# Performance work log

Hardware: AMD Instinct MI355X
Metric: run time of the kernel (lower is better)

## Reference

```python
import jax, jax.numpy as jnp
import numpy as np

B, N, D, H = 256, 196, 384, 1536  # batch, patches, dim, mlp hidden


def fake_quant(w, bits):
    """Symmetric per-tensor uniform fake quantization with straight-through estimator."""
    qmax = 2.0 ** (bits - 1) - 1.0
    scale = jnp.maximum(jnp.max(jnp.abs(w)) / qmax, 1e-8)
    q = jnp.clip(jnp.round(w / scale), -qmax, qmax) * scale
    return w + jax.lax.stop_gradient(q - w)


def setup_inputs() -> dict:
    key = jax.random.key(0)
    ks = jax.random.split(key, 8)
    return {
        "x": jax.random.normal(ks[0], (B, N, D), jnp.float32),
        "alpha1": jnp.ones((D,), jnp.float32),
        "beta1": jnp.zeros((D,), jnp.float32),
        "W_attn": jax.random.normal(ks[1], (N, N), jnp.float32) * (1.0 / np.sqrt(N)),
        "b_attn": jnp.zeros((N,), jnp.float32),
        "gamma1": jax.random.uniform(ks[2], (D,), jnp.float32) * 0.1,
        "alpha2": jnp.ones((D,), jnp.float32),
        "beta2": jnp.zeros((D,), jnp.float32),
        "W1": jax.random.normal(ks[3], (H, D), jnp.float32) * (1.0 / np.sqrt(D)),
        "b1": jnp.zeros((H,), jnp.float32),
        "W2": jax.random.normal(ks[4], (D, H), jnp.float32) * (1.0 / np.sqrt(H)),
        "b2": jnp.zeros((D,), jnp.float32),
        "gamma2": jax.random.uniform(ks[5], (D,), jnp.float32) * 0.1,
        "bits": 8,
    }


def reference(x, alpha1, beta1, W_attn, b_attn, gamma1,
              alpha2, beta2, W1, b1, W2, b2, gamma2, bits):
    # --- token-mixing branch ---
    org = x
    h = alpha1 * x + beta1                                   # Aff norm1, [B,N,D]
    # transpose(1,2) -> [B,D,N]; Linear(N,N); transpose back == einsum over patch dim
    Wq = fake_quant(W_attn, bits)
    h = jnp.einsum('bnd,mn->bmd', h, Wq) + b_attn[:, None]   # [B,N,D], bias per patch
    x = gamma1 * h + org                                     # layerscale + residual
    # --- channel-mixing branch ---
    org = x
    h = alpha2 * x + beta2                                   # Aff norm2
    h = jax.nn.gelu(h @ fake_quant(W1, bits).T + b1)         # [B,N,H]
    h = h @ fake_quant(W2, bits).T + b2                      # [B,N,D]
    return gamma2 * h + org
```

## Files before the change

kernel.cpp:

```cpp
#include <hip/hip_runtime.h>
#include <hip/hip_bf16.h>
#include <stdint.h>

#define Bb 256
#define Nn 196
#define Dd 384
#define Hh 1536
#define NPAD 224
#define MPAD 256
#define TTOT (Bb*Nn)
#define XLD 232
#define TK 64
#define HS 128

typedef __attribute__((ext_vector_type(8))) __bf16 bf16x8;
typedef __attribute__((ext_vector_type(4))) float f32x4;

#define GLD16(gp, lp) __builtin_amdgcn_global_load_lds( \
    (const __attribute__((address_space(1))) void*)(gp), \
    (__attribute__((address_space(3))) void*)(lp), 16, 0, 0)

#define MFMA16(a, b, c) __builtin_amdgcn_mfma_f32_16x16x32_bf16((a), (b), (c), 0, 0, 0)

__device__ __forceinline__ ushort f2bf(float f){
  union { float f; unsigned u; } v; v.f = f;
  unsigned r = v.u + 0x7FFFu + ((v.u >> 16) & 1u);
  return (ushort)(r >> 16);
}

__global__ void absmax3_k(const float* __restrict__ wa, const float* __restrict__ w1,
                          const float* __restrict__ w2, unsigned* __restrict__ out){
  int which = blockIdx.y;
  const float* w = which == 0 ? wa : (which == 1 ? w1 : w2);
  int n = which == 0 ? Nn*Nn : Hh*Dd;
  float m = 0.f;
  for (int i = blockIdx.x*blockDim.x + threadIdx.x; i < n; i += gridDim.x*blockDim.x)
    m = fmaxf(m, fabsf(w[i]));
  #pragma unroll
  for (int o = 32; o >= 1; o >>= 1) m = fmaxf(m, __shfl_xor(m, o));
  __shared__ float sm[4];
  if ((threadIdx.x & 63) == 0) sm[threadIdx.x >> 6] = m;
  __syncthreads();
  if (threadIdx.x == 0){
    float mm = fmaxf(fmaxf(sm[0], sm[1]), fmaxf(sm[2], sm[3]));
    atomicMax(out + which, __float_as_uint(mm));
  }
}

__global__ void quant_attn_k(const float* __restrict__ W, const unsigned* __restrict__ amax,
                             const int* __restrict__ bitsp, ushort* __restrict__ Wq){
  int idx = blockIdx.x*256 + threadIdx.x;
  int m = idx / NPAD, n = idx - m*NPAD;
  float qmax = (float)((1 << (bitsp[0]-1)) - 1);
  float s = fmaxf(__uint_as_float(amax[0]) / qmax, 1e-8f);
  float v = 0.f;
  if (m < Nn && n < Nn){
    float q = fminf(fmaxf(rintf(W[m*Nn + n] / s), -qmax), qmax);
    v = q * s;
  }
  Wq[idx] = f2bf(v);
}

__global__ void quant_k(const float* __restrict__ W, int n, const unsigned* __restrict__ amax,
                        const int* __restrict__ bitsp, ushort* __restrict__ Wq){
  int idx = blockIdx.x*256 + threadIdx.x;
  if (idx >= n) return;
  float qmax = (float)((1 << (bitsp[0]-1)) - 1);
  float s = fmaxf(__uint_as_float(amax[0]) / qmax, 1e-8f);
  float q = fminf(fmaxf(rintf(W[idx] / s), -qmax), qmax);
  Wq[idx] = f2bf(q * s);
}

__device__ __forceinline__ void stage_tile(const ushort* __restrict__ src, long ld, int k0,
                                           ushort* dst){
  const int tid = threadIdx.x;
  const long row = tid >> 2;
  const int  c8  = (tid & 3) * 8;
  GLD16(src + row*ld + k0 + c8,        dst + tid*8);
  GLD16(src + (row+64)*ld + k0 + c8,   dst + 2048 + tid*8);
}

__global__ __launch_bounds__(256) void gemm1_k(const ushort* __restrict__ Wq,
    const float* __restrict__ x,
    const float* __restrict__ alpha1, const float* __restrict__ beta1,
    const float* __restrict__ b_attn, const float* __restrict__ gamma1,
    const float* __restrict__ alpha2, const float* __restrict__ beta2,
    float* __restrict__ x1, ushort* __restrict__ hn2){
  __shared__ ushort Xs[128*XLD];
  __shared__ ushort BufAs[8192];
  const int tid = threadIdx.x;
  const int b = blockIdx.y, dt = blockIdx.x, d0 = dt*128;

  {
    float* buf = (float*)BufAs;
    const int dme = tid & 127;
    const float a1 = alpha1[d0 + dme], be1 = beta1[d0 + dme];
    for (int p = 0; p < 7; p++){
      __syncthreads();
      #pragma unroll
      for (int c = 0; c < 4; c++){
        int nn = p*32 + c*8 + (tid >> 5);
        int ncl = nn < Nn ? nn : Nn - 1;
        GLD16(x + ((long)b*Nn + ncl)*Dd + d0 + (tid & 31)*4,
              (char*)BufAs + c*4096 + tid*16);
      }
      __syncthreads();
      for (int g = tid >> 7; g < 4; g += 2){
        int n0 = g*8;
        ushort o[8];
        #pragma unroll
        for (int t = 0; t < 8; t++){
          int na = p*32 + n0 + t;
          float val = (na < Nn) ? fmaf(a1, buf[(n0 + t)*128 + dme], be1) : 0.f;
          o[t] = f2bf(val);
        }
        *(int4*)&Xs[dme*XLD + p*32 + n0] = *(int4*)o;
      }
    }
  }

  const int lane = tid & 63;
  const int wr = (tid >> 7) & 1, wc = (tid >> 6) & 1;
  const int arow = lane & 15, koff = (lane >> 4)*8;
  ushort* As = BufAs;
  for (int mt = 0; mt < 2; mt++){
    f32x4 acc[4][4] = {};
    const ushort* Wt = Wq + (long)mt*128*NPAD;
    for (int k0 = 0; k0 < NPAD; k0 += 32){
      __syncthreads();
      stage_tile(Wt, NPAD, k0, As);
      __syncthreads();
      bf16x8 ag[4], bg[4];
      #pragma unroll
      for (int i=0;i<4;i++){
        ag[i] = *(const bf16x8*)&As[(wr*64 + i*16 + arow)*32 + koff];
        bg[i] = *(const bf16x8*)&Xs[(wc*64 + i*16 + arow)*XLD + k0 + koff];
      }
      #pragma unroll
      for (int i=0;i<4;i++)
        #pragma unroll
        for (int j=0;j<4;j++)
          acc[i][j] = MFMA16(ag[i], bg[j], acc[i][j]);
    }
    #pragma unroll
    for (int i=0;i<4;i++){
      #pragma unroll
      for (int j=0;j<4;j++){
        int d = d0 + wc*64 + j*16 + (lane & 15);
        float g1 = gamma1[d], a2 = alpha2[d], b2v = beta2[d];
        #pragma unroll
        for (int r=0;r<4;r++){
          int m = mt*128 + wr*64 + i*16 + (lane >> 4)*4 + r;
          if (m < Nn){
            long idx = ((long)b*Nn + m)*Dd + d;
            float o = fmaf(g1, acc[i][j][r] + b_attn[m], x[idx]);
            x1[idx]  = o;
            hn2[idx] = f2bf(fmaf(a2, o, b2v));
          }
        }
      }
    }
  }
}


__device__ __forceinline__ void stage_a(const ushort* __restrict__ hn2, long t0, int k0,
                                        const ushort* __restrict__ W1q, int hs,
                                        ushort* As, ushort* W1s){
  const int tid = threadIdx.x;
  const int w = tid >> 6, lane = tid & 63;
  const int srcc = (((lane & 7) ^ ((lane >> 3) & 7))) * 8;
  const int rowa = w*8 + (lane >> 3);
  GLD16(hn2 + (t0 + rowa)*Dd + k0 + srcc,        As + (w*64 + lane)*8);
  GLD16(hn2 + (t0 + 32 + rowa)*Dd + k0 + srcc,   As + (256 + w*64 + lane)*8);
  #pragma unroll
  for (int q = 0; q < 4; q++){
    int row = q*32 + rowa;
    GLD16(W1q + ((long)hs*HS + row)*Dd + k0 + srcc, W1s + (q*256 + w*64 + lane)*8);
  }
}

__device__ __forceinline__ void stage_b(const ushort* __restrict__ W2q, int hcol0,
                                        ushort* W2s){
  const int tid = threadIdx.x;
  const int w = tid >> 6, lane = tid & 63;
  const int srcc = ((lane & 3) ^ ((lane >> 3) & 3)) * 8;
  #pragma unroll
  for (int q = 0; q < 6; q++){
    int row = q*64 + w*16 + (lane >> 2);
    GLD16(W2q + (long)row*Hh + hcol0 + srcc, W2s + (q*256 + w*64 + lane)*8);
  }
}

__global__ __launch_bounds__(256, 2) void mlp_k(const ushort* __restrict__ hn2,
    const ushort* __restrict__ W1q, const ushort* __restrict__ W2q,
    const float* __restrict__ b1, const float* __restrict__ b2,
    const float* __restrict__ gamma2, float* __restrict__ out){
  __shared__ ushort SH[36864];
  ushort* const AsP[2] = { SH, SH + 4096 };
  ushort* const Ps     = SH + 4096;
  ushort* const WsP[2] = { SH + 12288, SH + 24576 };

  const int tid  = threadIdx.x;
  const int lane = tid & 63;
  const int wv   = tid >> 6;
  const int arow = lane & 15;
  const int g    = lane >> 4;
  const long t0  = (long)blockIdx.x * TK;

  f32x4 oacc[4][6] = {};

  stage_a(hn2, t0, 0, W1q, 0, AsP[0], WsP[0]);
  __syncthreads();

  for (int hs = 0; hs < 12; hs++){
    f32x4 pacc[4][2] = {};
    #pragma unroll
    for (int ka = 0; ka < 6; ka++){
      const int cur = ka & 1;
      if (ka < 5) stage_a(hn2, t0, (ka+1)*64, W1q, hs, AsP[cur^1], WsP[cur^1]);
      else        stage_b(W2q, hs*HS, WsP[0]);
      const ushort* As  = AsP[cur];
      const ushort* W1s = WsP[cur];
      bf16x8 ag[4][2], bg[2][2];
      #pragma unroll
      for (int i=0;i<4;i++)
        #pragma unroll
        for (int ks=0;ks<2;ks++)
          ag[i][ks] = *(const bf16x8*)&As[(i*16 + arow)*64 + (((ks*4 + g) ^ (arow & 7))*8)];
      #pragma unroll
      for (int j=0;j<2;j++)
        #pragma unroll
        for (int ks=0;ks<2;ks++)
          bg[j][ks] = *(const bf16x8*)&W1s[(wv*32 + j*16 + arow)*64 + (((ks*4 + g) ^ (arow & 7))*8)];
      #pragma unroll
      for (int ks=0;ks<2;ks++)
        #pragma unroll
        for (int i=0;i<4;i++)
          #pragma unroll
          for (int j=0;j<2;j++)
            pacc[i][j] = MFMA16(ag[i][ks], bg[j][ks], pacc[i][j]);
      __syncthreads();
    }
    #pragma unroll
    for (int j=0;j<2;j++){
      int hcol = wv*32 + j*16 + arow;
      float b1v = b1[hs*HS + hcol];
      #pragma unroll
      for (int i=0;i<4;i++){
        #pragma unroll
        for (int r=0;r<4;r++){
          int row = i*16 + g*4 + r;
          float v = pacc[i][j][r] + b1v;
          float u = 0.7978845608028654f * v * fmaf(0.044715f, v*v, 1.f);
          float gl = v / (1.f + __expf(-2.f*u));
          Ps[row*128 + (hcol ^ ((row & 7) << 3))] = f2bf(gl);
        }
      }
    }
    __syncthreads();
    #pragma unroll
    for (int kb = 0; kb < 4; kb++){
      const int cur = kb & 1;
      if (kb < 3)       stage_b(W2q, hs*HS + (kb+1)*32, WsP[cur^1]);
      else if (hs < 11) stage_a(hn2, t0, 0, W1q, hs+1, AsP[0], WsP[0]);
      const ushort* W2s = WsP[cur];
      bf16x8 pa[4], bgb[6];
      #pragma unroll
      for (int i=0;i<4;i++){
        int row = i*16 + arow;
        pa[i] = *(const bf16x8*)&Ps[row*128 + ((kb*32 + g*8) ^ ((row & 7) << 3))];
      }
      #pragma unroll
      for (int j=0;j<6;j++){
        int row = wv*96 + j*16 + arow;
        bgb[j] = *(const bf16x8*)&W2s[row*32 + ((g ^ ((arow >> 1) & 3))*8)];
      }
      #pragma unroll
      for (int i=0;i<4;i++)
        #pragma unroll
        for (int j=0;j<6;j++)
          oacc[i][j] = MFMA16(pa[i], bgb[j], oacc[i][j]);
      __syncthreads();
    }
  }

  #pragma unroll
  for (int i=0;i<4;i++){
    #pragma unroll
    for (int j=0;j<6;j++){
      int d = wv*96 + j*16 + arow;
      float g2 = gamma2[d], b2v = b2[d];
      #pragma unroll
      for (int r=0;r<4;r++){
        long t = t0 + i*16 + g*4 + r;
        long idx = t*Dd + d;
        out[idx] = fmaf(g2, oacc[i][j][r] + b2v, out[idx]);
      }
    }
  }
}

extern "C" void kernel_launch(void* const* d_in, const int* in_sizes, int n_in,
                              void* d_out, int out_size, void* d_ws, size_t ws_size,
                              hipStream_t stream){
  const float* x      = (const float*)d_in[0];
  const float* alpha1 = (const float*)d_in[1];
  const float* beta1  = (const float*)d_in[2];
  const float* W_attn = (const float*)d_in[3];
  const float* b_attn = (const float*)d_in[4];
  const float* gamma1 = (const float*)d_in[5];
  const float* alpha2 = (const float*)d_in[6];
  const float* beta2  = (const float*)d_in[7];
  const float* W1     = (const float*)d_in[8];
  const float* b1     = (const float*)d_in[9];
  const float* W2     = (const float*)d_in[10];
  const float* b2     = (const float*)d_in[11];
  const float* gamma2 = (const float*)d_in[12];
  const int*   bits   = (const int*)d_in[13];

  char* ws = (char*)d_ws;
  unsigned* amax = (unsigned*)ws;
  ushort* Wq   = (ushort*)(ws + 256);
  ushort* W1q  = (ushort*)(ws + 114944);
  ushort* W2q  = (ushort*)(ws + 1294592);
  ushort* hn2  = (ushort*)(ws + 2474240);
  float*  x1   = (float*)d_out;

  hipMemsetAsync(amax, 0, 256, stream);
  absmax3_k<<<dim3(128, 3), 256, 0, stream>>>(W_attn, W1, W2, amax);
  quant_attn_k<<<(MPAD*NPAD)/256, 256, 0, stream>>>(W_attn, amax, bits, Wq);
  quant_k<<<(Hh*Dd)/256, 256, 0, stream>>>(W1, Hh*Dd, amax + 1, bits, W1q);
  quant_k<<<(Hh*Dd)/256, 256, 0, stream>>>(W2, Hh*Dd, amax + 2, bits, W2q);
  gemm1_k<<<dim3(3, Bb), 256, 0, stream>>>(Wq, x, alpha1, beta1, b_attn, gamma1,
                                           alpha2, beta2, x1, hn2);
  mlp_k<<<TTOT/TK, 256, 0, stream>>>(hn2, W1q, W2q, b1, b2, gamma2, (float*)d_out);
}
```

Before: 376.3 us.

## Deepen MLP pipeline with 3-slot LDS ring, 128-token tiles and 512 threads

Reworks the fused MLP kernel to process 128 tokens per block with 8 waves, a three-slot LDS ring buffer and partial vmcnt waits, so global-to-LDS loads run two stages ahead instead of syncing fully after each step. It also caches b1 in LDS, raises wave priority around MFMA bursts, and removes per-k shared-memory staging of Wq in gemm1 by reading Wq directly from global memory. The aim is more reuse of W1 and W2 across tokens and better overlap of loads with compute. The costs are higher LDS use per block, which limits occupancy, and fragile hand-written waitcnt counts.

```diff
diff --git a/kernel.cpp b/kernel.cpp
--- a/kernel.cpp
+++ b/kernel.cpp
@@ -10,7 +10,7 @@
 #define MPAD 256
 #define TTOT (Bb*Nn)
 #define XLD 232
-#define TK 64
+#define TK 128
 #define HS 128
 
 typedef __attribute__((ext_vector_type(8))) __bf16 bf16x8;
@@ -21,6 +21,9 @@
     (__attribute__((address_space(3))) void*)(lp), 16, 0, 0)
 
 #define MFMA16(a, b, c) __builtin_amdgcn_mfma_f32_16x16x32_bf16((a), (b), (c), 0, 0, 0)
+
+#define PHASE_SYNC   asm volatile("s_waitcnt vmcnt(4)\ns_barrier" ::: "memory")
+#define PHASE_SYNC_L asm volatile("s_waitcnt vmcnt(4) lgkmcnt(0)\ns_barrier" ::: "memory")
 
 __device__ __forceinline__ ushort f2bf(float f){
   union { float f; unsigned u; } v; v.f = f;
@@ -71,28 +74,18 @@
   Wq[idx] = f2bf(q * s);
 }
 
-__device__ __forceinline__ void stage_tile(const ushort* __restrict__ src, long ld, int k0,
-                                           ushort* dst){
-  const int tid = threadIdx.x;
-  const long row = tid >> 2;
-  const int  c8  = (tid & 3) * 8;
-  GLD16(src + row*ld + k0 + c8,        dst + tid*8);
-  GLD16(src + (row+64)*ld + k0 + c8,   dst + 2048 + tid*8);
-}
-
-__global__ __launch_bounds__(256) void gemm1_k(const ushort* __restrict__ Wq,
+__global__ __launch_bounds__(256, 2) void gemm1_k(const ushort* __restrict__ Wq,
     const float* __restrict__ x,
     const float* __restrict__ alpha1, const float* __restrict__ beta1,
     const float* __restrict__ b_attn, const float* __restrict__ gamma1,
     const float* __restrict__ alpha2, const float* __restrict__ beta2,
     float* __restrict__ x1, ushort* __restrict__ hn2){
   __shared__ ushort Xs[128*XLD];
-  __shared__ ushort BufAs[8192];
+  __shared__ float  Sbuf[32*128];
   const int tid = threadIdx.x;
   const int b = blockIdx.y, dt = blockIdx.x, d0 = dt*128;
 
   {
-    float* buf = (float*)BufAs;
     const int dme = tid & 127;
     const float a1 = alpha1[d0 + dme], be1 = beta1[d0 + dme];
     for (int p = 0; p < 7; p++){
@@ -102,7 +95,7 @@
         int nn = p*32 + c*8 + (tid >> 5);
         int ncl = nn < Nn ? nn : Nn - 1;
         GLD16(x + ((long)b*Nn + ncl)*Dd + d0 + (tid & 31)*4,
-              (char*)BufAs + c*4096 + tid*16);
+              (char*)Sbuf + c*4096 + tid*16);
       }
       __syncthreads();
       for (int g = tid >> 7; g < 4; g += 2){
@@ -111,30 +104,28 @@
         #pragma unroll
         for (int t = 0; t < 8; t++){
           int na = p*32 + n0 + t;
-          float val = (na < Nn) ? fmaf(a1, buf[(n0 + t)*128 + dme], be1) : 0.f;
+          float val = (na < Nn) ? fmaf(a1, Sbuf[(n0 + t)*128 + dme], be1) : 0.f;
           o[t] = f2bf(val);
         }
         *(int4*)&Xs[dme*XLD + p*32 + n0] = *(int4*)o;
       }
     }
   }
+  __syncthreads();
 
   const int lane = tid & 63;
   const int wr = (tid >> 7) & 1, wc = (tid >> 6) & 1;
   const int arow = lane & 15, koff = (lane >> 4)*8;
-  ushort* As = BufAs;
   for (int mt = 0; mt < 2; mt++){
     f32x4 acc[4][4] = {};
-    const ushort* Wt = Wq + (long)mt*128*NPAD;
-    for (int k0 = 0; k0 < NPAD; k0 += 32){
-      __syncthreads();
-      stage_tile(Wt, NPAD, k0, As);
-      __syncthreads();
+    #pragma unroll
+    for (int k7 = 0; k7 < 7; k7++){
       bf16x8 ag[4], bg[4];
       #pragma unroll
       for (int i=0;i<4;i++){
-        ag[i] = *(const bf16x8*)&As[(wr*64 + i*16 + arow)*32 + koff];
-        bg[i] = *(const bf16x8*)&Xs[(wc*64 + i*16 + arow)*XLD + k0 + koff];
+        int row = mt*128 + wr*64 + i*16 + arow;
+        ag[i] = *(const bf16x8*)&Wq[row*NPAD + k7*32 + koff];
+        bg[i] = *(const bf16x8*)&Xs[(wc*64 + i*16 + arow)*XLD + k7*32 + koff];
       }
       #pragma unroll
       for (int i=0;i<4;i++)
@@ -164,75 +155,83 @@
 }
 
 
-__device__ __forceinline__ void stage_a(const ushort* __restrict__ hn2, long t0, int k0,
-                                        const ushort* __restrict__ W1q, int hs,
-                                        ushort* As, ushort* W1s){
+__device__ __forceinline__ void stage_A(const ushort* __restrict__ hn2t,
+                                        const ushort* __restrict__ W1q, int hs, int ka,
+                                        ushort* slot){
   const int tid = threadIdx.x;
-  const int w = tid >> 6, lane = tid & 63;
-  const int srcc = (((lane & 7) ^ ((lane >> 3) & 7))) * 8;
-  const int rowa = w*8 + (lane >> 3);
-  GLD16(hn2 + (t0 + rowa)*Dd + k0 + srcc,        As + (w*64 + lane)*8);
-  GLD16(hn2 + (t0 + 32 + rowa)*Dd + k0 + srcc,   As + (256 + w*64 + lane)*8);
-  #pragma unroll
-  for (int q = 0; q < 4; q++){
-    int row = q*32 + rowa;
-    GLD16(W1q + ((long)hs*HS + row)*Dd + k0 + srcc, W1s + (q*256 + w*64 + lane)*8);
-  }
-}
-
-__device__ __forceinline__ void stage_b(const ushort* __restrict__ W2q, int hcol0,
-                                        ushort* W2s){
+  const int r0 = tid >> 3;
+  const int cs = ((tid & 7) ^ (r0 & 7)) * 8;
+  const int k0 = ka*64;
+  const ushort* w1 = W1q + (long)hs*HS*Dd + k0;
+  GLD16(hn2t + (long)r0*Dd + k0 + cs,        slot + tid*8);
+  GLD16(hn2t + (long)(r0+64)*Dd + k0 + cs,   slot + 4096 + tid*8);
+  GLD16(w1 + (long)r0*Dd + cs,               slot + 8192 + tid*8);
+  GLD16(w1 + (long)(r0+64)*Dd + cs,          slot + 12288 + tid*8);
+}
+
+__device__ __forceinline__ void stage_B(const ushort* __restrict__ W2q, int hs, int kb,
+                                        ushort* slot){
   const int tid = threadIdx.x;
-  const int w = tid >> 6, lane = tid & 63;
-  const int srcc = ((lane & 3) ^ ((lane >> 3) & 3)) * 8;
-  #pragma unroll
-  for (int q = 0; q < 6; q++){
-    int row = q*64 + w*16 + (lane >> 2);
-    GLD16(W2q + (long)row*Hh + hcol0 + srcc, W2s + (q*256 + w*64 + lane)*8);
-  }
-}
-
-__global__ __launch_bounds__(256, 2) void mlp_k(const ushort* __restrict__ hn2,
+  const int r = tid >> 2;
+  const int cs = ((tid & 3) ^ ((r >> 1) & 3)) * 8;
+  const ushort* w2 = W2q + hs*HS + kb*32;
+  GLD16(w2 + (long)r*Hh + cs,          slot + tid*8);
+  GLD16(w2 + (long)(r+128)*Hh + cs,    slot + 4096 + tid*8);
+  GLD16(w2 + (long)(r+256)*Hh + cs,    slot + 8192 + tid*8);
+  GLD16(w2 + (long)(r+384)*Hh + cs,    slot + 12288 + tid*8);
+}
+
+__global__ __launch_bounds__(512, 2) void mlp_k(const ushort* __restrict__ hn2,
     const ushort* __restrict__ W1q, const ushort* __restrict__ W2q,
     const float* __restrict__ b1, const float* __restrict__ b2,
     const float* __restrict__ gamma2, float* __restrict__ out){
-  __shared__ ushort SH[36864];
-  ushort* const AsP[2] = { SH, SH + 4096 };
-  ushort* const Ps     = SH + 4096;
-  ushort* const WsP[2] = { SH + 12288, SH + 24576 };
+  __shared__ ushort RING[3*16384];
+  __shared__ ushort Ps[TK*HS];
+  __shared__ float  b1s[Hh];
 
   const int tid  = threadIdx.x;
   const int lane = tid & 63;
   const int wv   = tid >> 6;
+  const int wt   = wv >> 2;
+  const int wh   = wv & 3;
   const int arow = lane & 15;
+  const int a7   = arow & 7;
   const int g    = lane >> 4;
   const long t0  = (long)blockIdx.x * TK;
+  const ushort* hn2t = hn2 + t0*Dd;
+
+  if (tid < 384) *(float4*)&b1s[tid*4] = *(const float4*)&b1[tid*4];
+
+  stage_A(hn2t, W1q, 0, 0, RING);
+  stage_A(hn2t, W1q, 0, 1, RING + 16384);
+  __syncthreads();
 
   f32x4 oacc[4][6] = {};
-
-  stage_a(hn2, t0, 0, W1q, 0, AsP[0], WsP[0]);
-  __syncthreads();
-
-  for (int hs = 0; hs < 12; hs++){
+  int cs = 0, ns = 2;
+
+  for (int hs = 0; hs < 12; ++hs){
+    const int hsn = (hs < 11) ? hs + 1 : 11;
     f32x4 pacc[4][2] = {};
     #pragma unroll
-    for (int ka = 0; ka < 6; ka++){
-      const int cur = ka & 1;
-      if (ka < 5) stage_a(hn2, t0, (ka+1)*64, W1q, hs, AsP[cur^1], WsP[cur^1]);
-      else        stage_b(W2q, hs*HS, WsP[0]);
-      const ushort* As  = AsP[cur];
-      const ushort* W1s = WsP[cur];
+    for (int p = 0; p < 6; ++p){
+      PHASE_SYNC;
+      ushort* st = RING + ns*16384;
+      if (p < 4) stage_A(hn2t, W1q, hs, p+2, st);
+      else       stage_B(W2q, hs, p-4, st);
+      const ushort* Asl = RING + cs*16384;
+      const ushort* W1l = Asl + 8192;
       bf16x8 ag[4][2], bg[2][2];
       #pragma unroll
-      for (int i=0;i<4;i++)
-        #pragma unroll
-        for (int ks=0;ks<2;ks++)
-          ag[i][ks] = *(const bf16x8*)&As[(i*16 + arow)*64 + (((ks*4 + g) ^ (arow & 7))*8)];
-      #pragma unroll
-      for (int j=0;j<2;j++)
-        #pragma unroll
-        for (int ks=0;ks<2;ks++)
-          bg[j][ks] = *(const bf16x8*)&W1s[(wv*32 + j*16 + arow)*64 + (((ks*4 + g) ^ (arow & 7))*8)];
+      for (int ks=0; ks<2; ks++){
+        const int cu8 = ((ks*4 + g) ^ a7) * 8;
+        #pragma unroll
+        for (int i=0;i<4;i++)
+          ag[i][ks] = *(const bf16x8*)&Asl[(wt*64 + i*16 + arow)*64 + cu8];
+        #pragma unroll
+        for (int j=0;j<2;j++)
+          bg[j][ks] = *(const bf16x8*)&W1l[(wh*32 + j*16 + arow)*64 + cu8];
+      }
+      __builtin_amdgcn_s_setprio(1);
       #pragma unroll
       for (int ks=0;ks<2;ks++)
         #pragma unroll
@@ -240,60 +239,64 @@
           #pragma unroll
           for (int j=0;j<2;j++)
             pacc[i][j] = MFMA16(ag[i][ks], bg[j][ks], pacc[i][j]);
-      __syncthreads();
+      __builtin_amdgcn_s_setprio(0);
+      cs = cs==2?0:cs+1; ns = ns==2?0:ns+1;
     }
     #pragma unroll
     for (int j=0;j<2;j++){
-      int hcol = wv*32 + j*16 + arow;
-      float b1v = b1[hs*HS + hcol];
+      int hcol = wh*32 + j*16 + arow;
+      float b1v = b1s[hs*HS + hcol];
       #pragma unroll
       for (int i=0;i<4;i++){
         #pragma unroll
         for (int r=0;r<4;r++){
-          int row = i*16 + g*4 + r;
+          int row = wt*64 + i*16 + g*4 + r;
           float v = pacc[i][j][r] + b1v;
           float u = 0.7978845608028654f * v * fmaf(0.044715f, v*v, 1.f);
           float gl = v / (1.f + __expf(-2.f*u));
-          Ps[row*128 + (hcol ^ ((row & 7) << 3))] = f2bf(gl);
+          Ps[row*HS + (hcol ^ ((row & 7) << 3))] = f2bf(gl);
         }
       }
     }
-    __syncthreads();
-    #pragma unroll
-    for (int kb = 0; kb < 4; kb++){
-      const int cur = kb & 1;
-      if (kb < 3)       stage_b(W2q, hs*HS + (kb+1)*32, WsP[cur^1]);
-      else if (hs < 11) stage_a(hn2, t0, 0, W1q, hs+1, AsP[0], WsP[0]);
-      const ushort* W2s = WsP[cur];
+    #pragma unroll
+    for (int p = 6; p < 10; ++p){
+      if (p == 6) { PHASE_SYNC_L; } else { PHASE_SYNC; }
+      ushort* st = RING + ns*16384;
+      if (p < 8) stage_B(W2q, hs, p-4, st);
+      else       stage_A(hn2t, W1q, hsn, p-8, st);
+      const ushort* W2l = RING + cs*16384;
+      const int kb = p - 6;
       bf16x8 pa[4], bgb[6];
       #pragma unroll
       for (int i=0;i<4;i++){
-        int row = i*16 + arow;
-        pa[i] = *(const bf16x8*)&Ps[row*128 + ((kb*32 + g*8) ^ ((row & 7) << 3))];
-      }
-      #pragma unroll
-      for (int j=0;j<6;j++){
-        int row = wv*96 + j*16 + arow;
-        bgb[j] = *(const bf16x8*)&W2s[row*32 + ((g ^ ((arow >> 1) & 3))*8)];
-      }
+        int row = wt*64 + i*16 + arow;
+        pa[i] = *(const bf16x8*)&Ps[row*HS + ((kb*32 + g*8) ^ (a7 << 3))];
+      }
+      const int u8 = (g ^ ((arow >> 1) & 3)) * 8;
+      #pragma unroll
+      for (int j=0;j<6;j++)
+        bgb[j] = *(const bf16x8*)&W2l[(wh*96 + j*16 + arow)*32 + u8];
+      __builtin_amdgcn_s_setprio(1);
       #pragma unroll
       for (int i=0;i<4;i++)
         #pragma unroll
         for (int j=0;j<6;j++)
           oacc[i][j] = MFMA16(pa[i], bgb[j], oacc[i][j]);
-      __syncthreads();
-    }
-  }
+      __builtin_amdgcn_s_setprio(0);
+      cs = cs==2?0:cs+1; ns = ns==2?0:ns+1;
+    }
+  }
+  asm volatile("s_waitcnt vmcnt(0)" ::: "memory");
 
   #pragma unroll
   for (int i=0;i<4;i++){
     #pragma unroll
     for (int j=0;j<6;j++){
-      int d = wv*96 + j*16 + arow;
+      int d = wh*96 + j*16 + arow;
       float g2 = gamma2[d], b2v = b2[d];
       #pragma unroll
       for (int r=0;r<4;r++){
-        long t = t0 + i*16 + g*4 + r;
+        long t = t0 + wt*64 + i*16 + g*4 + r;
         long idx = t*Dd + d;
         out[idx] = fmaf(g2, oacc[i][j][r] + b2v, out[idx]);
       }
@@ -324,7 +327,7 @@
   ushort* Wq   = (ushort*)(ws + 256);
   ushort* W1q  = (ushort*)(ws + 114944);
   ushort* W2q  = (ushort*)(ws + 1294592);
-  ushort* hn2  = (ushort*)(ws + 2474240);
+  ushort* hn2  = (ushort*)(ws + 2867456);
   float*  x1   = (float*)d_out;
 
   hipMemsetAsync(amax, 0, 256, stream);
@@ -334,5 +337,5 @@
   quant_k<<<(Hh*Dd)/256, 256, 0, stream>>>(W2, Hh*Dd, amax + 2, bits, W2q);
   gemm1_k<<<dim3(3, Bb), 256, 0, stream>>>(Wq, x, alpha1, beta1, b_attn, gamma1,
                                            alpha2, beta2, x1, hn2);
-  mlp_k<<<TTOT/TK, 256, 0, stream>>>(hn2, W1q, W2q, b1, b2, gamma2, (float*)d_out);
-}
+  mlp_k<<<TTOT/TK, 512, 0, stream>>>(hn2, W1q, W2q, b1, b2, gamma2, (float*)d_out);
+}
```

Result: slower. 414.5 us (+10.2%).
